# Kernel optimization log

Measured on AMD Instinct MI355X. Metric: run time of the kernel, lower is better.

The kernel has to match this reference:

```python
import jax, jax.numpy as jnp
import numpy as np

N, E = 100000, 1600000
F_IN, H, C = 128, 64, 16
BN_EPS = 1e-5


def setup_inputs() -> dict:
    key = jax.random.key(0)
    ks = jax.random.split(key, 10)
    def w(k, shape):
        fan_in = shape[0]
        return (jax.random.normal(k, shape, dtype=jnp.float32) / np.sqrt(fan_in)).astype(jnp.float32)
    return {
        "x": jax.random.normal(ks[0], (N, F_IN), dtype=jnp.float32),
        "edge_index": jax.random.randint(ks[1], (2, E), 0, N, dtype=jnp.int32),
        "W1": w(ks[2], (F_IN, H)), "b1": jnp.zeros((H,), jnp.float32),
        "g1": jnp.ones((H,), jnp.float32), "be1": jnp.zeros((H,), jnp.float32),
        "W2": w(ks[3], (H, H)), "b2": jnp.zeros((H,), jnp.float32),
        "W3": w(ks[4], (H, H)), "b3": jnp.zeros((H,), jnp.float32),
        "g2": jnp.ones((H,), jnp.float32), "be2": jnp.zeros((H,), jnp.float32),
        "W4": w(ks[5], (H, H)), "b4": jnp.zeros((H,), jnp.float32),
        "Wl1": w(ks[6], (2 * H, H)), "bl1": jnp.zeros((H,), jnp.float32),
        "Wl2": w(ks[7], (H, C)), "bl2": jnp.zeros((C,), jnp.float32),
    }


def _gin_layer(h, src, dst, Wa, ba, g, be, Wb, bb):
    # GINConv (eps=0): mlp((1+0)*x_i + sum_{j->i} x_j)
    agg = jax.ops.segment_sum(h[src], dst, num_segments=h.shape[0])  # [N, F]
    z = (h + agg) @ Wa + ba
    # BatchNorm1d (training-mode batch stats, biased variance)
    mu = jnp.mean(z, axis=0)
    var = jnp.mean((z - mu) ** 2, axis=0)
    z = (z - mu) * jax.lax.rsqrt(var + BN_EPS) * g + be
    z = jax.nn.elu(z)
    return jax.nn.elu(z @ Wb + bb)


def reference(x, edge_index, W1, b1, g1, be1, W2, b2, W3, b3, g2, be2, W4, b4, Wl1, bl1, Wl2, bl2):
    src, dst = edge_index[0], edge_index[1]
    h1 = _gin_layer(x, src, dst, W1, b1, g1, be1, W2, b2)   # [N, H]
    h2 = _gin_layer(h1, src, dst, W3, b3, g2, be2, W4, b4)  # [N, H]
    h = jnp.concatenate([h1, h2], axis=1)                    # [N, 2H]
    h = jax.nn.relu(h @ Wl1 + bl1)
    # dropout is identity at inference
    return h @ Wl2 + bl2                                     # [N, C]
```

## Files before the change

### kernel.cpp

```cpp
#include <hip/hip_runtime.h>
#include <hip/hip_bf16.h>
#include <stddef.h>

constexpr int N    = 100000;
constexpr int E    = 1600000;
constexpr int F_IN = 128;
constexpr int H    = 64;
constexpr int C    = 16;
constexpr float BN_EPS = 1e-5f;

constexpr int TILE  = 128;
constexpr int NB    = (N + TILE - 1) / TILE;
constexpr int CAP   = 2816;
constexpr int CHUNK = 8192;
constexpr int FBLK  = (E + CHUNK - 1) / CHUNK;

#define DEV __device__ __forceinline__

DEV float elu_f(float x) { return x > 0.f ? x : (expf(x) - 1.f); }

__global__ void k_initcur(int* __restrict__ gcur) {
    int i = threadIdx.x + blockIdx.x * blockDim.x;
    if (i < NB) gcur[i] = i * CAP;
}

__global__ __launch_bounds__(256) void k_binfill(const int* __restrict__ esrc,
                                                 const int* __restrict__ edst,
                                                 int* __restrict__ gcur,
                                                 int* __restrict__ ebuf) {
    __shared__ int lcnt[NB];
    __shared__ int lbase[NB];
    const int t    = threadIdx.x;
    const int cbeg = blockIdx.x * CHUNK;
    const int cend = (cbeg + CHUNK < E) ? cbeg + CHUNK : E;

    for (int i = t; i < NB; i += 256) lcnt[i] = 0;
    __syncthreads();
    for (int i = cbeg + t; i < cend; i += 256)
        atomicAdd(&lcnt[edst[i] >> 7], 1);
    __syncthreads();
    for (int i = t; i < NB; i += 256) {
        int c = lcnt[i];
        lbase[i] = c ? atomicAdd(&gcur[i], c) : 0;
    }
    __syncthreads();
    for (int i = t; i < NB; i += 256) lcnt[i] = 0;
    __syncthreads();
    for (int i = cbeg + t; i < cend; i += 256) {
        int d = edst[i], s = esrc[i];
        int b = d >> 7;
        int pos = lbase[b] + atomicAdd(&lcnt[b], 1);
        ebuf[pos] = s | ((d & (TILE - 1)) << 17);
    }
}

__global__ __launch_bounds__(1024) void k_bscan(const int* __restrict__ gcur,
                                                int* __restrict__ bbase,
                                                int* __restrict__ row_ptr) {
    __shared__ int sc[1024];
    int t = threadIdx.x;
    int cnt = (t < NB) ? (gcur[t] - t * CAP) : 0;
    sc[t] = cnt;
    __syncthreads();
    for (int off = 1; off < 1024; off <<= 1) {
        int v = (t >= off) ? sc[t - off] : 0;
        __syncthreads();
        sc[t] += v;
        __syncthreads();
    }
    if (t < NB) bbase[t] = sc[t] - cnt;
    if (t == 0) row_ptr[N] = E;
}

__global__ __launch_bounds__(256) void k_bsort(const int* __restrict__ ebuf,
                                               const int* __restrict__ gcur,
                                               const int* __restrict__ bbase,
                                               int* __restrict__ row_ptr,
                                               int* __restrict__ csr_src) {
    __shared__ int hist[TILE];
    __shared__ int sc[TILE];
    __shared__ int cur[TILE];
    const int t   = threadIdx.x;
    const int b   = blockIdx.x;
    const int beg = b * CAP;
    const int cnt = gcur[b] - beg;
    const int gb  = bbase[b];

    if (t < TILE) hist[t] = 0;
    __syncthreads();
    for (int i = t; i < cnt; i += 256)
        atomicAdd(&hist[(ebuf[beg + i] >> 17) & (TILE - 1)], 1);
    __syncthreads();
    if (t < TILE) sc[t] = hist[t];
    __syncthreads();
    for (int off = 1; off < TILE; off <<= 1) {
        int v = (t < TILE && t >= off) ? sc[t - off] : 0;
        __syncthreads();
        if (t < TILE) sc[t] += v;
        __syncthreads();
    }
    if (t < TILE) {
        int excl = sc[t] - hist[t];
        cur[t] = excl;
        int gn = b * TILE + t;
        if (gn < N) row_ptr[gn] = gb + excl;
    }
    __syncthreads();
    for (int i = t; i < cnt; i += 256) {
        int pack = ebuf[beg + i];
        int dl   = (pack >> 17) & (TILE - 1);
        int pos  = gb + atomicAdd(&cur[dl], 1);
        csr_src[pos] = pack & 0x1FFFF;
    }
}

__global__ __launch_bounds__(256) void k_agg(const float* __restrict__ y,
                                             const int* __restrict__ row_ptr,
                                             const int* __restrict__ csr_src,
                                             const float* __restrict__ bias,
                                             float* __restrict__ z) {
    int wid  = (blockIdx.x * blockDim.x + threadIdx.x) >> 6;
    int lane = threadIdx.x & 63;
    if (wid >= N) return;
    float self = y[(size_t)wid * 64 + lane];
    int beg = __builtin_amdgcn_readfirstlane(row_ptr[wid]);
    int end = __builtin_amdgcn_readfirstlane(row_ptr[wid + 1]);
    int deg = end - beg;
    int myidx = (lane < deg) ? csr_src[beg + lane] : 0;

    float acc = self + bias[lane];
    int d64 = deg < 64 ? deg : 64;
    int k = 0;
    for (; k + 8 <= d64; k += 8) {
        int s0 = __shfl(myidx, k + 0);
        int s1 = __shfl(myidx, k + 1);
        int s2 = __shfl(myidx, k + 2);
        int s3 = __shfl(myidx, k + 3);
        int s4 = __shfl(myidx, k + 4);
        int s5 = __shfl(myidx, k + 5);
        int s6 = __shfl(myidx, k + 6);
        int s7 = __shfl(myidx, k + 7);
        float v0 = y[(size_t)s0 * 64 + lane];
        float v1 = y[(size_t)s1 * 64 + lane];
        float v2 = y[(size_t)s2 * 64 + lane];
        float v3 = y[(size_t)s3 * 64 + lane];
        float v4 = y[(size_t)s4 * 64 + lane];
        float v5 = y[(size_t)s5 * 64 + lane];
        float v6 = y[(size_t)s6 * 64 + lane];
        float v7 = y[(size_t)s7 * 64 + lane];
        acc += v0; acc += v1; acc += v2; acc += v3;
        acc += v4; acc += v5; acc += v6; acc += v7;
    }
    for (; k < d64; ++k) {
        int s = __shfl(myidx, k);
        acc += y[(size_t)s * 64 + lane];
    }
    for (int kk = beg + 64; kk < end; ++kk) {
        int s = csr_src[kk];
        acc += y[(size_t)s * 64 + lane];
    }
    z[(size_t)wid * 64 + lane] = acc;
}

__global__ __launch_bounds__(256) void k_stats1(const float* __restrict__ z,
                                                float* __restrict__ part) {
    __shared__ float s1[256], s2[256];
    int t = threadIdx.x;
    int f = t & 63, g = t >> 6;
    float sum = 0.f, sq = 0.f;
    for (int r = blockIdx.x * 4 + g; r < N; r += gridDim.x * 4) {
        float v = z[(size_t)r * 64 + f];
        sum += v;
        sq  += v * v;
    }
    s1[t] = sum; s2[t] = sq;
    __syncthreads();
    if (t < 128) { s1[t] += s1[t + 128]; s2[t] += s2[t + 128]; }
    __syncthreads();
    if (t < 64) {
        part[blockIdx.x * 128 + t]      = s1[t] + s1[t + 64];
        part[blockIdx.x * 128 + 64 + t] = s2[t] + s2[t + 64];
    }
}

__global__ void k_stats2(const float* __restrict__ part, const float* __restrict__ g,
                         const float* __restrict__ be, float* __restrict__ scale,
                         float* __restrict__ shift) {
    __shared__ float lds[128];
    int t = threadIdx.x;
    float s = 0.f;
    for (int b = 0; b < 256; ++b) s += part[b * 128 + t];
    lds[t] = s;
    __syncthreads();
    if (t < 64) {
        float mu   = lds[t] * (1.f / N);
        float var  = lds[64 + t] * (1.f / N) - mu * mu;
        float rstd = rsqrtf(var + BN_EPS);
        float sc   = rstd * g[t];
        scale[t] = sc;
        shift[t] = be[t] - mu * sc;
    }
}

template <int K, bool BN_IN, bool ELU_OUT, bool BIAS>
__global__ __launch_bounds__(256) void k_linear(const float* __restrict__ in,
                                                const float* __restrict__ W,
                                                const float* __restrict__ bias,
                                                const float* __restrict__ scale,
                                                const float* __restrict__ shift,
                                                float* __restrict__ out) {
    const int lane = threadIdx.x & 63;
    const int wid  = (blockIdx.x * blockDim.x + threadIdx.x) >> 6;
    const int row  = wid * 64 + lane;
    if (row >= N) return;

    float acc[64];
#pragma unroll
    for (int f = 0; f < 64; ++f) acc[f] = BIAS ? bias[f] : 0.f;

    const float* xr = in + (size_t)row * K;

#pragma unroll 2
    for (int k4 = 0; k4 < K / 4; ++k4) {
        float4 xv = *reinterpret_cast<const float4*>(xr + k4 * 4);
        if (BN_IN) {
            const int c = k4 * 4;
            xv.x = elu_f(xv.x * scale[c + 0] + shift[c + 0]);
            xv.y = elu_f(xv.y * scale[c + 1] + shift[c + 1]);
            xv.z = elu_f(xv.z * scale[c + 2] + shift[c + 2]);
            xv.w = elu_f(xv.w * scale[c + 3] + shift[c + 3]);
        }
#pragma unroll
        for (int j = 0; j < 4; ++j) {
            const float xk = (j == 0) ? xv.x : (j == 1) ? xv.y : (j == 2) ? xv.z : xv.w;
            const float4* Wk = reinterpret_cast<const float4*>(W + (size_t)(k4 * 4 + j) * 64);
#pragma unroll
            for (int f4 = 0; f4 < 16; ++f4) {
                float4 w = Wk[f4];
                acc[f4 * 4 + 0] = fmaf(xk, w.x, acc[f4 * 4 + 0]);
                acc[f4 * 4 + 1] = fmaf(xk, w.y, acc[f4 * 4 + 1]);
                acc[f4 * 4 + 2] = fmaf(xk, w.z, acc[f4 * 4 + 2]);
                acc[f4 * 4 + 3] = fmaf(xk, w.w, acc[f4 * 4 + 3]);
            }
        }
    }

    float* orow = out + (size_t)row * 64;
#pragma unroll
    for (int f4 = 0; f4 < 16; ++f4) {
        float4 v;
        v.x = ELU_OUT ? elu_f(acc[f4 * 4 + 0]) : acc[f4 * 4 + 0];
        v.y = ELU_OUT ? elu_f(acc[f4 * 4 + 1]) : acc[f4 * 4 + 1];
        v.z = ELU_OUT ? elu_f(acc[f4 * 4 + 2]) : acc[f4 * 4 + 2];
        v.w = ELU_OUT ? elu_f(acc[f4 * 4 + 3]) : acc[f4 * 4 + 3];
        *reinterpret_cast<float4*>(orow + f4 * 4) = v;
    }
}

__global__ __launch_bounds__(256) void k_final(const float* __restrict__ h1,
                                               const float* __restrict__ h2,
                                               const float* __restrict__ Wl1,
                                               const float* __restrict__ bl1,
                                               const float* __restrict__ Wl2,
                                               const float* __restrict__ bl2,
                                               float* __restrict__ out) {
    const int lane = threadIdx.x & 63;
    const int wid  = (blockIdx.x * blockDim.x + threadIdx.x) >> 6;
    const int row  = wid * 64 + lane;
    if (row >= N) return;

    float acc[64];
#pragma unroll
    for (int f = 0; f < 64; ++f) acc[f] = bl1[f];

#pragma unroll 1
    for (int half = 0; half < 2; ++half) {
        const float* xr = (half == 0 ? h1 : h2) + (size_t)row * 64;
        const float* Wh = Wl1 + (size_t)half * 64 * 64;
#pragma unroll 2
        for (int k4 = 0; k4 < 16; ++k4) {
            float4 xv = *reinterpret_cast<const float4*>(xr + k4 * 4);
#pragma unroll
            for (int j = 0; j < 4; ++j) {
                const float xk = (j == 0) ? xv.x : (j == 1) ? xv.y : (j == 2) ? xv.z : xv.w;
                const float4* Wk = reinterpret_cast<const float4*>(Wh + (size_t)(k4 * 4 + j) * 64);
#pragma unroll
                for (int f4 = 0; f4 < 16; ++f4) {
                    float4 w = Wk[f4];
                    acc[f4 * 4 + 0] = fmaf(xk, w.x, acc[f4 * 4 + 0]);
                    acc[f4 * 4 + 1] = fmaf(xk, w.y, acc[f4 * 4 + 1]);
                    acc[f4 * 4 + 2] = fmaf(xk, w.z, acc[f4 * 4 + 2]);
                    acc[f4 * 4 + 3] = fmaf(xk, w.w, acc[f4 * 4 + 3]);
                }
            }
        }
    }

    float acc2[16];
#pragma unroll
    for (int c = 0; c < 16; ++c) acc2[c] = bl2[c];
#pragma unroll
    for (int k = 0; k < 64; ++k) {
        float tk = fmaxf(acc[k], 0.f);
        const float4* Wk = reinterpret_cast<const float4*>(Wl2 + (size_t)k * 16);
#pragma unroll
        for (int c4 = 0; c4 < 4; ++c4) {
            float4 w = Wk[c4];
            acc2[c4 * 4 + 0] = fmaf(tk, w.x, acc2[c4 * 4 + 0]);
            acc2[c4 * 4 + 1] = fmaf(tk, w.y, acc2[c4 * 4 + 1]);
            acc2[c4 * 4 + 2] = fmaf(tk, w.z, acc2[c4 * 4 + 2]);
            acc2[c4 * 4 + 3] = fmaf(tk, w.w, acc2[c4 * 4 + 3]);
        }
    }

    float* orow = out + (size_t)row * 16;
#pragma unroll
    for (int c4 = 0; c4 < 4; ++c4) {
        float4 v;
        v.x = acc2[c4 * 4 + 0];
        v.y = acc2[c4 * 4 + 1];
        v.z = acc2[c4 * 4 + 2];
        v.w = acc2[c4 * 4 + 3];
        *reinterpret_cast<float4*>(orow + c4 * 4) = v;
    }
}

extern "C" void kernel_launch(void* const* d_in, const int* in_sizes, int n_in,
                              void* d_out, int out_size, void* d_ws, size_t ws_size,
                              hipStream_t stream) {
    const float* x   = (const float*)d_in[0];
    const int*   ei  = (const int*)d_in[1];
    const int*   esrc = ei;
    const int*   edst = ei + E;
    const float* W1  = (const float*)d_in[2];
    const float* b1  = (const float*)d_in[3];
    const float* g1  = (const float*)d_in[4];
    const float* be1 = (const float*)d_in[5];
    const float* W2  = (const float*)d_in[6];
    const float* b2  = (const float*)d_in[7];
    const float* W3  = (const float*)d_in[8];
    const float* b3  = (const float*)d_in[9];
    const float* g2  = (const float*)d_in[10];
    const float* be2 = (const float*)d_in[11];
    const float* W4  = (const float*)d_in[12];
    const float* b4  = (const float*)d_in[13];
    const float* Wl1 = (const float*)d_in[14];
    const float* bl1 = (const float*)d_in[15];
    const float* Wl2 = (const float*)d_in[16];
    const float* bl2 = (const float*)d_in[17];
    float* out = (float*)d_out;

    char* p = (char*)d_ws;
    auto carve = [&](size_t bytes) {
        void* r = (void*)p;
        p += (bytes + 255) & ~(size_t)255;
        return r;
    };
    constexpr size_t SROW = (size_t)N * H * sizeof(float);
    float* y   = (float*)carve(SROW);
    float* z   = (float*)carve(SROW);
    float* h1  = (float*)carve(SROW);
    float* h2  = (float*)carve(SROW);
    int*   ebuf    = (int*)carve((size_t)NB * CAP * 4);
    int*   gcur    = (int*)carve((size_t)NB * 4);
    int*   bbase   = (int*)carve((size_t)NB * 4);
    int*   row_ptr = (int*)carve((size_t)(N + 1) * 4);
    int*   csr     = (int*)carve((size_t)E * 4);
    float* part    = (float*)carve((size_t)256 * 128 * 4);
    float* scale   = (float*)carve(64 * 4);
    float* shift   = (float*)carve(64 * 4);
    (void)ws_size; (void)in_sizes; (void)n_in; (void)out_size;

    constexpr int LINB = ((N + 63) / 64 + 3) / 4;
    constexpr int AGGB = (N * 64 + 255) / 256;

    k_initcur<<<1, 1024, 0, stream>>>(gcur);
    k_binfill<<<FBLK, 256, 0, stream>>>(esrc, edst, gcur, ebuf);
    k_bscan<<<1, 1024, 0, stream>>>(gcur, bbase, row_ptr);
    k_bsort<<<NB, 256, 0, stream>>>(ebuf, gcur, bbase, row_ptr, csr);

    k_linear<128, false, false, false><<<LINB, 256, 0, stream>>>(x, W1, nullptr, nullptr, nullptr, y);
    k_agg<<<AGGB, 256, 0, stream>>>(y, row_ptr, csr, b1, z);
    k_stats1<<<256, 256, 0, stream>>>(z, part);
    k_stats2<<<1, 128, 0, stream>>>(part, g1, be1, scale, shift);
    k_linear<64, true, true, true><<<LINB, 256, 0, stream>>>(z, W2, b2, scale, shift, h1);

    k_linear<64, false, false, false><<<LINB, 256, 0, stream>>>(h1, W3, nullptr, nullptr, nullptr, y);
    k_agg<<<AGGB, 256, 0, stream>>>(y, row_ptr, csr, b3, z);
    k_stats1<<<256, 256, 0, stream>>>(z, part);
    k_stats2<<<1, 128, 0, stream>>>(part, g2, be2, scale, shift);
    k_linear<64, true, true, true><<<LINB, 256, 0, stream>>>(z, W4, b4, scale, shift, h2);

    k_final<<<LINB, 256, 0, stream>>>(h1, h2, Wl1, bl1, Wl2, bl2, out);
}
```

Baseline: 581.0 us.

## Split dense-layer rows across four threads and widen BN stats grid

Each row of the linear and final kernels is now handled by four threads, each computing 16 of the 64 output columns, with a shuffle reduction for the second final-layer matmul. The goal is lower register pressure and four times as many threads for latency hiding, at the cost of four threads each reading the same input row and some shuffle overhead. The BN statistics kernel grid also grows from 256 to 1024 blocks, so the single-block second stage must sum more partials.

```diff
diff --git a/kernel.cpp b/kernel.cpp
--- a/kernel.cpp
+++ b/kernel.cpp
@@ -14,6 +14,8 @@
 constexpr int CAP   = 2816;
 constexpr int CHUNK = 8192;
 constexpr int FBLK  = (E + CHUNK - 1) / CHUNK;
+
+constexpr int SGRID = 1024;
 
 #define DEV __device__ __forceinline__
 
@@ -189,7 +191,7 @@
     __shared__ float lds[128];
     int t = threadIdx.x;
     float s = 0.f;
-    for (int b = 0; b < 256; ++b) s += part[b * 128 + t];
+    for (int b = 0; b < SGRID; ++b) s += part[(size_t)b * 128 + t];
     lds[t] = s;
     __syncthreads();
     if (t < 64) {
@@ -209,16 +211,17 @@
                                                 const float* __restrict__ scale,
                                                 const float* __restrict__ shift,
                                                 float* __restrict__ out) {
-    const int lane = threadIdx.x & 63;
-    const int wid  = (blockIdx.x * blockDim.x + threadIdx.x) >> 6;
-    const int row  = wid * 64 + lane;
+    const int tid = blockIdx.x * blockDim.x + threadIdx.x;
+    const int row = tid >> 2;
+    const int g   = tid & 3;
     if (row >= N) return;
 
-    float acc[64];
-#pragma unroll
-    for (int f = 0; f < 64; ++f) acc[f] = BIAS ? bias[f] : 0.f;
+    float acc[16];
+#pragma unroll
+    for (int f = 0; f < 16; ++f) acc[f] = BIAS ? bias[g * 16 + f] : 0.f;
 
     const float* xr = in + (size_t)row * K;
+    const float* Wg = W + g * 16;
 
 #pragma unroll 2
     for (int k4 = 0; k4 < K / 4; ++k4) {
@@ -233,9 +236,9 @@
 #pragma unroll
         for (int j = 0; j < 4; ++j) {
             const float xk = (j == 0) ? xv.x : (j == 1) ? xv.y : (j == 2) ? xv.z : xv.w;
-            const float4* Wk = reinterpret_cast<const float4*>(W + (size_t)(k4 * 4 + j) * 64);
-#pragma unroll
-            for (int f4 = 0; f4 < 16; ++f4) {
+            const float4* Wk = reinterpret_cast<const float4*>(Wg + (size_t)(k4 * 4 + j) * 64);
+#pragma unroll
+            for (int f4 = 0; f4 < 4; ++f4) {
                 float4 w = Wk[f4];
                 acc[f4 * 4 + 0] = fmaf(xk, w.x, acc[f4 * 4 + 0]);
                 acc[f4 * 4 + 1] = fmaf(xk, w.y, acc[f4 * 4 + 1]);
@@ -245,9 +248,9 @@
         }
     }
 
-    float* orow = out + (size_t)row * 64;
-#pragma unroll
-    for (int f4 = 0; f4 < 16; ++f4) {
+    float* orow = out + (size_t)row * 64 + g * 16;
+#pragma unroll
+    for (int f4 = 0; f4 < 4; ++f4) {
         float4 v;
         v.x = ELU_OUT ? elu_f(acc[f4 * 4 + 0]) : acc[f4 * 4 + 0];
         v.y = ELU_OUT ? elu_f(acc[f4 * 4 + 1]) : acc[f4 * 4 + 1];
@@ -264,19 +267,19 @@
                                                const float* __restrict__ Wl2,
                                                const float* __restrict__ bl2,
                                                float* __restrict__ out) {
-    const int lane = threadIdx.x & 63;
-    const int wid  = (blockIdx.x * blockDim.x + threadIdx.x) >> 6;
-    const int row  = wid * 64 + lane;
+    const int tid = blockIdx.x * blockDim.x + threadIdx.x;
+    const int row = tid >> 2;
+    const int g   = tid & 3;
     if (row >= N) return;
 
-    float acc[64];
-#pragma unroll
-    for (int f = 0; f < 64; ++f) acc[f] = bl1[f];
+    float acc[16];
+#pragma unroll
+    for (int f = 0; f < 16; ++f) acc[f] = bl1[g * 16 + f];
 
 #pragma unroll 1
     for (int half = 0; half < 2; ++half) {
         const float* xr = (half == 0 ? h1 : h2) + (size_t)row * 64;
-        const float* Wh = Wl1 + (size_t)half * 64 * 64;
+        const float* Wh = Wl1 + (size_t)half * 64 * 64 + g * 16;
 #pragma unroll 2
         for (int k4 = 0; k4 < 16; ++k4) {
             float4 xv = *reinterpret_cast<const float4*>(xr + k4 * 4);
@@ -285,7 +288,7 @@
                 const float xk = (j == 0) ? xv.x : (j == 1) ? xv.y : (j == 2) ? xv.z : xv.w;
                 const float4* Wk = reinterpret_cast<const float4*>(Wh + (size_t)(k4 * 4 + j) * 64);
 #pragma unroll
-                for (int f4 = 0; f4 < 16; ++f4) {
+                for (int f4 = 0; f4 < 4; ++f4) {
                     float4 w = Wk[f4];
                     acc[f4 * 4 + 0] = fmaf(xk, w.x, acc[f4 * 4 + 0]);
                     acc[f4 * 4 + 1] = fmaf(xk, w.y, acc[f4 * 4 + 1]);
@@ -298,11 +301,11 @@
 
     float acc2[16];
 #pragma unroll
-    for (int c = 0; c < 16; ++c) acc2[c] = bl2[c];
-#pragma unroll
-    for (int k = 0; k < 64; ++k) {
+    for (int c = 0; c < 16; ++c) acc2[c] = (g == 0) ? bl2[c] : 0.f;
+#pragma unroll
+    for (int k = 0; k < 16; ++k) {
         float tk = fmaxf(acc[k], 0.f);
-        const float4* Wk = reinterpret_cast<const float4*>(Wl2 + (size_t)k * 16);
+        const float4* Wk = reinterpret_cast<const float4*>(Wl2 + (size_t)(g * 16 + k) * 16);
 #pragma unroll
         for (int c4 = 0; c4 < 4; ++c4) {
             float4 w = Wk[c4];
@@ -313,16 +316,18 @@
         }
     }
 
-    float* orow = out + (size_t)row * 16;
-#pragma unroll
-    for (int c4 = 0; c4 < 4; ++c4) {
-        float4 v;
-        v.x = acc2[c4 * 4 + 0];
-        v.y = acc2[c4 * 4 + 1];
-        v.z = acc2[c4 * 4 + 2];
-        v.w = acc2[c4 * 4 + 3];
-        *reinterpret_cast<float4*>(orow + c4 * 4) = v;
-    }
+#pragma unroll
+    for (int c = 0; c < 16; ++c) {
+        acc2[c] += __shfl_xor(acc2[c], 1);
+        acc2[c] += __shfl_xor(acc2[c], 2);
+    }
+
+    float4 v;
+    if (g == 0)      v = float4{acc2[0],  acc2[1],  acc2[2],  acc2[3]};
+    else if (g == 1) v = float4{acc2[4],  acc2[5],  acc2[6],  acc2[7]};
+    else if (g == 2) v = float4{acc2[8],  acc2[9],  acc2[10], acc2[11]};
+    else             v = float4{acc2[12], acc2[13], acc2[14], acc2[15]};
+    *reinterpret_cast<float4*>(out + (size_t)row * 16 + g * 4) = v;
 }
 
 extern "C" void kernel_launch(void* const* d_in, const int* in_sizes, int n_in,
@@ -366,30 +371,30 @@
     int*   bbase   = (int*)carve((size_t)NB * 4);
     int*   row_ptr = (int*)carve((size_t)(N + 1) * 4);
     int*   csr     = (int*)carve((size_t)E * 4);
-    float* part    = (float*)carve((size_t)256 * 128 * 4);
+    float* part    = (float*)carve((size_t)SGRID * 128 * 4);
     float* scale   = (float*)carve(64 * 4);
     float* shift   = (float*)carve(64 * 4);
     (void)ws_size; (void)in_sizes; (void)n_in; (void)out_size;
 
-    constexpr int LINB = ((N + 63) / 64 + 3) / 4;
-    constexpr int AGGB = (N * 64 + 255) / 256;
+    constexpr int LIN4B = (N * 4 + 255) / 256;
+    constexpr int AGGB  = (N * 64 + 255) / 256;
 
     k_initcur<<<1, 1024, 0, stream>>>(gcur);
     k_binfill<<<FBLK, 256, 0, stream>>>(esrc, edst, gcur, ebuf);
     k_bscan<<<1, 1024, 0, stream>>>(gcur, bbase, row_ptr);
     k_bsort<<<NB, 256, 0, stream>>>(ebuf, gcur, bbase, row_ptr, csr);
 
-    k_linear<128, false, false, false><<<LINB, 256, 0, stream>>>(x, W1, nullptr, nullptr, nullptr, y);
+    k_linear<128, false, false, false><<<LIN4B, 256, 0, stream>>>(x, W1, nullptr, nullptr, nullptr, y);
     k_agg<<<AGGB, 256, 0, stream>>>(y, row_ptr, csr, b1, z);
-    k_stats1<<<256, 256, 0, stream>>>(z, part);
+    k_stats1<<<SGRID, 256, 0, stream>>>(z, part);
     k_stats2<<<1, 128, 0, stream>>>(part, g1, be1, scale, shift);
-    k_linear<64, true, true, true><<<LINB, 256, 0, stream>>>(z, W2, b2, scale, shift, h1);
-
-    k_linear<64, false, false, false><<<LINB, 256, 0, stream>>>(h1, W3, nullptr, nullptr, nullptr, y);
+    k_linear<64, true, true, true><<<LIN4B, 256, 0, stream>>>(z, W2, b2, scale, shift, h1);
+
+    k_linear<64, false, false, false><<<LIN4B, 256, 0, stream>>>(h1, W3, nullptr, nullptr, nullptr, y);
     k_agg<<<AGGB, 256, 0, stream>>>(y, row_ptr, csr, b3, z);
-    k_stats1<<<256, 256, 0, stream>>>(z, part);
+    k_stats1<<<SGRID, 256, 0, stream>>>(z, part);
     k_stats2<<<1, 128, 0, stream>>>(part, g2, be2, scale, shift);
-    k_linear<64, true, true, true><<<LINB, 256, 0, stream>>>(z, W4, b4, scale, shift, h2);
-
-    k_final<<<LINB, 256, 0, stream>>>(h1, h2, Wl1, bl1, Wl2, bl2, out);
-}
+    k_linear<64, true, true, true><<<LIN4B, 256, 0, stream>>>(z, W4, b4, scale, shift, h2);
+
+    k_final<<<LIN4B, 256, 0, stream>>>(h1, h2, Wl1, bl1, Wl2, bl2, out);
+}
```

Measured after the change: 1.126 ms. 93.8% more time.
